# Optimization experiments

Hardware: AMD Instinct MI355X
Metric: run time of the kernel (lower is better)

Reference implementation:

```python
import jax, jax.numpy as jnp
import numpy as np

T = 100000
M = 32
PI_CONST = 3.1415926  # matches the constant used in the original source


def setup_inputs() -> dict:
    key = jax.random.key(0)
    k1, k2, k3, k4, k5, k6 = jax.random.split(key, 6)
    obs_2_T = jax.random.normal(k1, (T,), dtype=jnp.float32)
    obs_1_T_1 = jax.random.normal(k2, (T,), dtype=jnp.float32)
    mean = jax.random.normal(k3, (M,), dtype=jnp.float32)
    # variances must be positive
    var = jax.random.uniform(k4, (M,), dtype=jnp.float32) + jnp.float32(0.5)
    bate = jnp.float32(0.85)
    # pi: valid initial distribution; aij: row-stochastic transition matrix
    pi = jax.nn.softmax(jax.random.normal(k5, (M,), dtype=jnp.float32))
    aij = jax.nn.softmax(jax.random.normal(k6, (M, M), dtype=jnp.float32), axis=-1)
    return {"obs_2_T": obs_2_T, "obs_1_T_1": obs_1_T_1, "mean": mean,
            "var": var, "bate": bate, "pi": pi, "aij": aij}


def reference(obs_2_T, obs_1_T_1, mean, var, bate, pi, aij):
    # Eta[i, j, t] = exp(-(obs2[t] - (mean[j] + bate*(obs1[t] - mean[i]))) / (2*var[j]))
    #               / sqrt(2*pi*var[j])
    # (NOTE: faithful to the source, which does NOT square the residual.)
    inv2v = 1.0 / (2.0 * var)                      # (m,)
    norm = 1.0 / jnp.sqrt(2.0 * PI_CONST * var)    # (m,)
    # diff: (m_i, m_j, T)
    diff = obs_2_T[None, None, :] - (mean[None, :, None]
                                     + bate * (obs_1_T_1[None, None, :] - mean[:, None, None]))
    Eta = jnp.exp(-diff * inv2v[None, :, None]) * norm[None, :, None]  # (m, m, T)
    Eta_t = jnp.moveaxis(Eta, -1, 0)  # (T, m, m)

    # Normalized forward recursion:
    # t=0: num[i,j] = Eta[i,j,0] * pi[i] * aij[i,j]
    # t>0: num[i,j] = Eta[i,j,t] * Epsilon[t-1,i] * aij[i,j]
    # Gamma[t] = num / sum(num);  Epsilon[t,j] = sum_i Gamma[t,i,j]
    def step(eps_prev, eta):  # eps_prev: (m,), eta: (m, m)
        num = eta * eps_prev[:, None] * aij
        g = num / jnp.sum(num)
        return jnp.sum(g, axis=0), g

    _, Gamma = jax.lax.scan(step, pi, Eta_t)  # Gamma: (T, m, m)

    # loss = sum_t <Gamma[t], Eta[:, :, t]>
    loss = jnp.sum(Gamma * Eta_t)
    return loss
```

## Files before the change

### kernel.cpp

```cpp
#include <hip/hip_runtime.h>

constexpr int TN   = 100000;
constexpr int NCH  = 2000;
constexpr int CLEN = 50;
constexpr int WARM = 12;
constexpr int WPB  = 4;
constexpr int NBLK = NCH / WPB;
constexpr int MAXS = WARM + CLEN;

constexpr float LOG2E = 1.4426950408889634f;
constexpr float PI_F  = 3.1415926f;

typedef float v2f __attribute__((ext_vector_type(2)));

#define ROR(src, N) __int_as_float(__builtin_amdgcn_mov_dpp( \
    __float_as_int(src), 0x120 + (N), 0xF, 0xF, false))

#define RING16(v) { v += ROR(v,1); v += ROR(v,2); v += ROR(v,4); v += ROR(v,8); }

#define ROTPAIRS(SRC, P)                                                      \
  v2f P[8];                                                                   \
  { P[0] = (v2f){SRC,        ROR(SRC,1)};  P[1] = (v2f){ROR(SRC,2),  ROR(SRC,3)};  \
    P[2] = (v2f){ROR(SRC,4), ROR(SRC,5)};  P[3] = (v2f){ROR(SRC,6),  ROR(SRC,7)};  \
    P[4] = (v2f){ROR(SRC,8), ROR(SRC,9)};  P[5] = (v2f){ROR(SRC,10), ROR(SRC,11)}; \
    P[6] = (v2f){ROR(SRC,12),ROR(SRC,13)}; P[7] = (v2f){ROR(SRC,14), ROR(SRC,15)}; }

#define PKDOT(Wp, P, dd)                                                      \
  float dd;                                                                   \
  { v2f a0 = Wp[0]*P[0], a1 = Wp[1]*P[1], a2 = Wp[2]*P[2], a3 = Wp[3]*P[3];   \
    a0 += Wp[4]*P[4]; a1 += Wp[5]*P[5]; a2 += Wp[6]*P[6]; a3 += Wp[7]*P[7];   \
    v2f b = (a0 + a1) + (a2 + a3);                                            \
    dd = b.x + b.y; }

__global__ __launch_bounds__(256, 5) void k_main(
    const float* __restrict__ obs2, const float* __restrict__ obs1,
    const float* __restrict__ mean_p, const float* __restrict__ var_p,
    const float* __restrict__ bate_p, const float* __restrict__ pi_p,
    const float* __restrict__ aij, float* __restrict__ out)
{
  const int w = threadIdx.x >> 6, lane = threadIdx.x & 63;
  const int wv = blockIdx.x * WPB + w;
  const int i  = lane & 15;
  const int b4 = (lane >> 4) & 1;
  const int h  = lane >> 5;
  const int j  = lane & 31;
  const int kb = h * 16;
  const int m  = kb + i;
  const int idx1 = m, idx2 = m + 32;

  __shared__ __align__(16) float Wsh[2][32][32];
  __shared__ float cts[WPB][MAXS + 4];
  __shared__ float bsum[WPB];

  {
    const int tid = threadIdx.x;
    const int jj = tid & 31, ig = tid >> 5;
    float vjq  = var_p[jj];
    float i2vq = 0.5f / vjq;
    float norm = rsqrtf(2.0f * PI_F * vjq);
    float Aj   = norm * expf(mean_p[jj] * i2vq);
    float bate = bate_p[0];
#pragma unroll
    for (int mm = 0; mm < 4; ++mm) {
      int ii = ig * 4 + mm;
      float Bij = expf(-bate * mean_p[ii] * i2vq);
      float wq = aij[ii * 32 + jj] * Aj * Bij;
      Wsh[0][ii][jj] = wq;
      Wsh[1][ii][jj] = wq * Aj * Bij;
    }
  }

  float i2v_j = 0.5f / var_p[j];
  float s_ = i2v_j;
#pragma unroll
  for (int o = 1; o < 32; o <<= 1) s_ += __shfl_xor(s_, o);
  const float mbar    = s_ * 0.03125f;
  const float slope_m = (0.5f / var_p[m] - mbar) * LOG2E;
  const float Mc      = mbar * LOG2E;

  const int t0 = wv * CLEN;
  const int tw = (t0 > WARM) ? (t0 - WARM) : 0;
  const int n  = t0 + CLEN - tw;
  const int warmsteps = t0 - tw;
  {
    float bate = bate_p[0];
    for (int l = lane; l < n; l += 64)
      cts[w][l] = obs2[tw + l] - bate * obs1[tw + l];
  }
  __syncthreads();

  int dird;
  { int p = __builtin_amdgcn_mov_dpp(i, 0x121, 0xF, 0xF, false);
    dird = (p - i) & 15; }

  v2f Wp[8], Vp[8];
#pragma unroll
  for (int N = 0; N < 8; ++N) {
    int k0 = (i + (2 * N)     * dird) & 15;
    int k1 = (i + (2 * N + 1) * dird) & 15;
    Wp[N] = (v2f){Wsh[0][kb + k0][j], Wsh[0][kb + k1][j]};
    Vp[N] = (v2f){Wsh[1][kb + k0][j], Wsh[1][kb + k1][j]};
  }

  float ysrc = (tw == 0) ? pi_p[m] : 0.03125f;

  for (int s = 0; s < warmsteps; ++s) {
    float ct = cts[w][s];
    float uB = exp2f(-ct * slope_m);
    ROTPAIRS(ysrc, P)
    PKDOT(Wp, P, pW)
    float bA = __shfl(pW, idx1);
    float bB = __shfl(pW, idx2);
    ysrc = uB * (bA + bB);
    if ((s & 7) == 7)
      ysrc *= __builtin_amdgcn_rcpf(__int_as_float(
                __builtin_amdgcn_readfirstlane(__float_as_int(ysrc))));
  }
  float lossacc = 0.f;
#pragma unroll 4
  for (int q = 0; q < CLEN; ++q) {
    float ct   = cts[w][warmsteps + q];
    float uB   = exp2f(-ct * slope_m);
    float corr = exp2f(-ct * Mc);
    ROTPAIRS(ysrc, P)
    PKDOT(Wp, P, pW)
    PKDOT(Vp, P, pV)
    float bA = __shfl(pW, idx1);
    float bB = __shfl(pW, idx2);
    float cA = __shfl(pV, idx1);
    float cB = __shfl(pV, idx2);
    float ynew = uB * (bA + bB);
    float vV   = (uB * uB) * (cA + cB);
    ysrc = ynew;
    if ((q & 7) == 7)
      ysrc *= __builtin_amdgcn_rcpf(__int_as_float(
                __builtin_amdgcn_readfirstlane(__float_as_int(ysrc))));
    float red = b4 ? vV : ynew;
    RING16(red)
    red += __shfl_xor(red, 32);
    float cross = __shfl_xor(red, 16);
    float S  = b4 ? cross : red;
    float N2 = b4 ? red   : cross;
    lossacc += corr * N2 * __builtin_amdgcn_rcpf(S);
  }
  if (lane == 0) bsum[w] = lossacc;
  __syncthreads();
  if (threadIdx.x == 0)
    atomicAdd(out, (bsum[0] + bsum[1]) + (bsum[2] + bsum[3]));
}

extern "C" void kernel_launch(void* const* d_in, const int* in_sizes, int n_in,
                              void* d_out, int out_size, void* d_ws, size_t ws_size,
                              hipStream_t stream)
{
  (void)in_sizes; (void)n_in; (void)ws_size; (void)d_ws;
  const float* obs2 = (const float*)d_in[0];
  const float* obs1 = (const float*)d_in[1];
  const float* mean = (const float*)d_in[2];
  const float* var  = (const float*)d_in[3];
  const float* bate = (const float*)d_in[4];
  const float* pi   = (const float*)d_in[5];
  const float* aij  = (const float*)d_in[6];
  float* out = (float*)d_out;

  hipMemsetAsync(out, 0, sizeof(float) * out_size, stream);
  k_main<<<NBLK, 256, 0, stream>>>(obs2, obs1, mean, var, bate, pi, aij, out);
}
```

Before: 107.3 us.

## Interleave two independent time chunks per wave for ILP in forward recursion

Splits the sequence into twice as many shorter chunks and has each wave advance two independent chunks at once, so the serial shuffle/DPP dependency chains of one chunk can overlap with the other. The final cross-half reduction now uses readlane to scalar registers instead of two shuffles. Launch bounds drop to two blocks per CU minimum, allowing more registers per thread. Shorter chunks mean the warm-up steps make up a larger share of total work, and there are half as many waves to hide latency.

```diff
diff --git a/kernel.cpp b/kernel.cpp
--- a/kernel.cpp
+++ b/kernel.cpp
@@ -1,11 +1,13 @@
 #include <hip/hip_runtime.h>
 
 constexpr int TN   = 100000;
-constexpr int NCH  = 2000;
-constexpr int CLEN = 50;
+constexpr int NCH  = 4000;
+constexpr int CLEN = 25;
 constexpr int WARM = 12;
+constexpr int ILP  = 2;
+constexpr int NWAVE = NCH / ILP;
 constexpr int WPB  = 4;
-constexpr int NBLK = NCH / WPB;
+constexpr int NBLK = NWAVE / WPB;
 constexpr int MAXS = WARM + CLEN;
 
 constexpr float LOG2E = 1.4426950408889634f;
@@ -17,6 +19,11 @@
     __float_as_int(src), 0x120 + (N), 0xF, 0xF, false))
 
 #define RING16(v) { v += ROR(v,1); v += ROR(v,2); v += ROR(v,4); v += ROR(v,8); }
+
+#define RDL(x, L) __int_as_float(__builtin_amdgcn_readlane(__float_as_int(x), (L)))
+
+#define RENORM(y) y *= __builtin_amdgcn_rcpf(__int_as_float( \
+    __builtin_amdgcn_readfirstlane(__float_as_int(y))));
 
 #define ROTPAIRS(SRC, P)                                                      \
   v2f P[8];                                                                   \
@@ -32,7 +39,7 @@
     v2f b = (a0 + a1) + (a2 + a3);                                            \
     dd = b.x + b.y; }
 
-__global__ __launch_bounds__(256, 5) void k_main(
+__global__ __launch_bounds__(256, 2) void k_main(
     const float* __restrict__ obs2, const float* __restrict__ obs1,
     const float* __restrict__ mean_p, const float* __restrict__ var_p,
     const float* __restrict__ bate_p, const float* __restrict__ pi_p,
@@ -49,7 +56,7 @@
   const int idx1 = m, idx2 = m + 32;
 
   __shared__ __align__(16) float Wsh[2][32][32];
-  __shared__ float cts[WPB][MAXS + 4];
+  __shared__ float cts[WPB][ILP][MAXS + 3];
   __shared__ float bsum[WPB];
 
   {
@@ -78,14 +85,20 @@
   const float slope_m = (0.5f / var_p[m] - mbar) * LOG2E;
   const float Mc      = mbar * LOG2E;
 
-  const int t0 = wv * CLEN;
-  const int tw = (t0 > WARM) ? (t0 - WARM) : 0;
-  const int n  = t0 + CLEN - tw;
-  const int warmsteps = t0 - tw;
+  const int cA = wv,            cB = wv + NWAVE;
+  const int t0A = cA * CLEN,    t0B = cB * CLEN;
+  const int twA = (t0A > WARM) ? (t0A - WARM) : 0;
+  const int twB = t0B - WARM;
+  const int wsA = t0A - twA;
+  const int nA  = t0A + CLEN - twA;
+  const int nB  = WARM + CLEN;
+
   {
     float bate = bate_p[0];
-    for (int l = lane; l < n; l += 64)
-      cts[w][l] = obs2[tw + l] - bate * obs1[tw + l];
+    for (int l = lane; l < nA; l += 64)
+      cts[w][0][l] = obs2[twA + l] - bate * obs1[twA + l];
+    for (int l = lane; l < nB; l += 64)
+      cts[w][1][l] = obs2[twB + l] - bate * obs1[twB + l];
   }
   __syncthreads();
 
@@ -102,46 +115,65 @@
     Vp[N] = (v2f){Wsh[1][kb + k0][j], Wsh[1][kb + k1][j]};
   }
 
-  float ysrc = (tw == 0) ? pi_p[m] : 0.03125f;
-
-  for (int s = 0; s < warmsteps; ++s) {
-    float ct = cts[w][s];
-    float uB = exp2f(-ct * slope_m);
-    ROTPAIRS(ysrc, P)
-    PKDOT(Wp, P, pW)
-    float bA = __shfl(pW, idx1);
-    float bB = __shfl(pW, idx2);
-    ysrc = uB * (bA + bB);
-    if ((s & 7) == 7)
-      ysrc *= __builtin_amdgcn_rcpf(__int_as_float(
-                __builtin_amdgcn_readfirstlane(__float_as_int(ysrc))));
-  }
+  float ysA = (twA == 0) ? pi_p[m] : 0.03125f;
+  float ysB = 0.03125f;
+
+  for (int s = 0; s < WARM; ++s) {
+    if (wsA) {
+      float ct = cts[w][0][s];
+      float uB = exp2f(-ct * slope_m);
+      ROTPAIRS(ysA, PA)
+      PKDOT(Wp, PA, pW)
+      float a1 = __shfl(pW, idx1);
+      float a2 = __shfl(pW, idx2);
+      ysA = uB * (a1 + a2);
+      if ((s & 7) == 7) { RENORM(ysA) }
+    }
+    {
+      float ct = cts[w][1][s];
+      float uB = exp2f(-ct * slope_m);
+      ROTPAIRS(ysB, PB)
+      PKDOT(Wp, PB, pW)
+      float a1 = __shfl(pW, idx1);
+      float a2 = __shfl(pW, idx2);
+      ysB = uB * (a1 + a2);
+      if ((s & 7) == 7) { RENORM(ysB) }
+    }
+  }
+
   float lossacc = 0.f;
-#pragma unroll 4
+#pragma unroll 5
   for (int q = 0; q < CLEN; ++q) {
-    float ct   = cts[w][warmsteps + q];
-    float uB   = exp2f(-ct * slope_m);
-    float corr = exp2f(-ct * Mc);
-    ROTPAIRS(ysrc, P)
-    PKDOT(Wp, P, pW)
-    PKDOT(Vp, P, pV)
-    float bA = __shfl(pW, idx1);
-    float bB = __shfl(pW, idx2);
-    float cA = __shfl(pV, idx1);
-    float cB = __shfl(pV, idx2);
-    float ynew = uB * (bA + bB);
-    float vV   = (uB * uB) * (cA + cB);
-    ysrc = ynew;
-    if ((q & 7) == 7)
-      ysrc *= __builtin_amdgcn_rcpf(__int_as_float(
-                __builtin_amdgcn_readfirstlane(__float_as_int(ysrc))));
-    float red = b4 ? vV : ynew;
-    RING16(red)
-    red += __shfl_xor(red, 32);
-    float cross = __shfl_xor(red, 16);
-    float S  = b4 ? cross : red;
-    float N2 = b4 ? red   : cross;
-    lossacc += corr * N2 * __builtin_amdgcn_rcpf(S);
+    float ctA = cts[w][0][wsA + q];
+    float ctB = cts[w][1][WARM + q];
+    float uBA = exp2f(-ctA * slope_m), corrA = exp2f(-ctA * Mc);
+    float uBB = exp2f(-ctB * slope_m), corrB = exp2f(-ctB * Mc);
+    ROTPAIRS(ysA, PA)
+    ROTPAIRS(ysB, PB)
+    PKDOT(Wp, PA, pWA)
+    PKDOT(Vp, PA, pVA)
+    PKDOT(Wp, PB, pWB)
+    PKDOT(Vp, PB, pVB)
+    float bA1 = __shfl(pWA, idx1), bA2 = __shfl(pWA, idx2);
+    float cA1 = __shfl(pVA, idx1), cA2 = __shfl(pVA, idx2);
+    float bB1 = __shfl(pWB, idx1), bB2 = __shfl(pWB, idx2);
+    float cB1 = __shfl(pVB, idx1), cB2 = __shfl(pVB, idx2);
+    float ynA = uBA * (bA1 + bA2);
+    float vVA = (uBA * uBA) * (cA1 + cA2);
+    float ynB = uBB * (bB1 + bB2);
+    float vVB = (uBB * uBB) * (cB1 + cB2);
+    ysA = ynA; ysB = ynB;
+    if ((q & 7) == 7) { RENORM(ysA) RENORM(ysB) }
+    float redA = b4 ? vVA : ynA;
+    RING16(redA)
+    float SAv  = RDL(redA, 0)  + RDL(redA, 32);
+    float N2Av = RDL(redA, 16) + RDL(redA, 48);
+    lossacc += corrA * N2Av * __builtin_amdgcn_rcpf(SAv);
+    float redB = b4 ? vVB : ynB;
+    RING16(redB)
+    float SBv  = RDL(redB, 0)  + RDL(redB, 32);
+    float N2Bv = RDL(redB, 16) + RDL(redB, 48);
+    lossacc += corrB * N2Bv * __builtin_amdgcn_rcpf(SBv);
   }
   if (lane == 0) bsum[w] = lossacc;
   __syncthreads();
```

Result: faster. 90.59 us (-15.6%).

## Halve chunk length, double chunks, and reduce sums via readlane scalars

Applied to the files above, without the earlier changes.

Splits the time series into twice as many chunks of half the length, so each wavefront runs a shorter serial recursion and there are more wavefronts in flight. It replaces the final xor shuffles with readlane-based scalar sums, lowers launch-bounds occupancy from 5 to 4, and swaps the weight arrays for named scalar vector registers. The cost is that the fixed 12-step warmup is now spent on half as much useful work, adding redundant computation, and lower allowed occupancy may reduce latency hiding.

```diff
diff --git a/kernel.cpp b/kernel.cpp
--- a/kernel.cpp
+++ b/kernel.cpp
@@ -1,8 +1,8 @@
 #include <hip/hip_runtime.h>
 
 constexpr int TN   = 100000;
-constexpr int NCH  = 2000;
-constexpr int CLEN = 50;
+constexpr int NCH  = 4000;
+constexpr int CLEN = 25;
 constexpr int WARM = 12;
 constexpr int WPB  = 4;
 constexpr int NBLK = NCH / WPB;
@@ -18,21 +18,32 @@
 
 #define RING16(v) { v += ROR(v,1); v += ROR(v,2); v += ROR(v,4); v += ROR(v,8); }
 
-#define ROTPAIRS(SRC, P)                                                      \
-  v2f P[8];                                                                   \
-  { P[0] = (v2f){SRC,        ROR(SRC,1)};  P[1] = (v2f){ROR(SRC,2),  ROR(SRC,3)};  \
-    P[2] = (v2f){ROR(SRC,4), ROR(SRC,5)};  P[3] = (v2f){ROR(SRC,6),  ROR(SRC,7)};  \
-    P[4] = (v2f){ROR(SRC,8), ROR(SRC,9)};  P[5] = (v2f){ROR(SRC,10), ROR(SRC,11)}; \
-    P[6] = (v2f){ROR(SRC,12),ROR(SRC,13)}; P[7] = (v2f){ROR(SRC,14), ROR(SRC,15)}; }
+#define RDL(x, L) __int_as_float(__builtin_amdgcn_readlane(__float_as_int(x), (L)))
 
-#define PKDOT(Wp, P, dd)                                                      \
-  float dd;                                                                   \
-  { v2f a0 = Wp[0]*P[0], a1 = Wp[1]*P[1], a2 = Wp[2]*P[2], a3 = Wp[3]*P[3];   \
-    a0 += Wp[4]*P[4]; a1 += Wp[5]*P[5]; a2 += Wp[6]*P[6]; a3 += Wp[7]*P[7];   \
-    v2f b = (a0 + a1) + (a2 + a3);                                            \
-    dd = b.x + b.y; }
+#define RENORM(y) y *= __builtin_amdgcn_rcpf(__int_as_float( \
+    __builtin_amdgcn_readfirstlane(__float_as_int(y))));
 
-__global__ __launch_bounds__(256, 5) void k_main(
+#define ROTPAIRS8(SRC, p0,p1,p2,p3,p4,p5,p6,p7)                               \
+  v2f p0 = (v2f){SRC,         ROR(SRC,1)};                                    \
+  v2f p1 = (v2f){ROR(SRC,2),  ROR(SRC,3)};                                    \
+  v2f p2 = (v2f){ROR(SRC,4),  ROR(SRC,5)};                                    \
+  v2f p3 = (v2f){ROR(SRC,6),  ROR(SRC,7)};                                    \
+  v2f p4 = (v2f){ROR(SRC,8),  ROR(SRC,9)};                                    \
+  v2f p5 = (v2f){ROR(SRC,10), ROR(SRC,11)};                                   \
+  v2f p6 = (v2f){ROR(SRC,12), ROR(SRC,13)};                                   \
+  v2f p7 = (v2f){ROR(SRC,14), ROR(SRC,15)};
+
+static __device__ __forceinline__ float pkdot8(
+    v2f w0, v2f w1, v2f w2, v2f w3, v2f w4, v2f w5, v2f w6, v2f w7,
+    v2f p0, v2f p1, v2f p2, v2f p3, v2f p4, v2f p5, v2f p6, v2f p7)
+{
+  v2f a0 = w0*p0, a1 = w1*p1, a2 = w2*p2, a3 = w3*p3;
+  a0 += w4*p4; a1 += w5*p5; a2 += w6*p6; a3 += w7*p7;
+  v2f b = (a0 + a1) + (a2 + a3);
+  return b.x + b.y;
+}
+
+__global__ __launch_bounds__(256, 4) void k_main(
     const float* __restrict__ obs2, const float* __restrict__ obs1,
     const float* __restrict__ mean_p, const float* __restrict__ var_p,
     const float* __restrict__ bate_p, const float* __restrict__ pi_p,
@@ -49,7 +60,7 @@
   const int idx1 = m, idx2 = m + 32;
 
   __shared__ __align__(16) float Wsh[2][32][32];
-  __shared__ float cts[WPB][MAXS + 4];
+  __shared__ float cts[WPB][MAXS + 3];
   __shared__ float bsum[WPB];
 
   {
@@ -93,38 +104,42 @@
   { int p = __builtin_amdgcn_mov_dpp(i, 0x121, 0xF, 0xF, false);
     dird = (p - i) & 15; }
 
-  v2f Wp[8], Vp[8];
-#pragma unroll
-  for (int N = 0; N < 8; ++N) {
-    int k0 = (i + (2 * N)     * dird) & 15;
-    int k1 = (i + (2 * N + 1) * dird) & 15;
-    Wp[N] = (v2f){Wsh[0][kb + k0][j], Wsh[0][kb + k1][j]};
-    Vp[N] = (v2f){Wsh[1][kb + k0][j], Wsh[1][kb + k1][j]};
-  }
+  v2f w0, w1, w2, w3, w4, w5, w6, w7;
+  v2f q0, q1, q2, q3, q4, q5, q6, q7;
+#define LDW(N, WV, QV) {                                                      \
+    int k0 = (i + (2 * (N))     * dird) & 15;                                 \
+    int k1 = (i + (2 * (N) + 1) * dird) & 15;                                 \
+    WV = (v2f){Wsh[0][kb + k0][j], Wsh[0][kb + k1][j]};                       \
+    QV = (v2f){Wsh[1][kb + k0][j], Wsh[1][kb + k1][j]}; }
+  LDW(0, w0, q0) LDW(1, w1, q1) LDW(2, w2, q2) LDW(3, w3, q3)
+  LDW(4, w4, q4) LDW(5, w5, q5) LDW(6, w6, q6) LDW(7, w7, q7)
+#undef LDW
 
   float ysrc = (tw == 0) ? pi_p[m] : 0.03125f;
 
   for (int s = 0; s < warmsteps; ++s) {
     float ct = cts[w][s];
     float uB = exp2f(-ct * slope_m);
-    ROTPAIRS(ysrc, P)
-    PKDOT(Wp, P, pW)
-    float bA = __shfl(pW, idx1);
-    float bB = __shfl(pW, idx2);
-    ysrc = uB * (bA + bB);
-    if ((s & 7) == 7)
-      ysrc *= __builtin_amdgcn_rcpf(__int_as_float(
-                __builtin_amdgcn_readfirstlane(__float_as_int(ysrc))));
+    ROTPAIRS8(ysrc, p0, p1, p2, p3, p4, p5, p6, p7)
+    float pW = pkdot8(w0, w1, w2, w3, w4, w5, w6, w7,
+                      p0, p1, p2, p3, p4, p5, p6, p7);
+    float a1 = __shfl(pW, idx1);
+    float a2 = __shfl(pW, idx2);
+    ysrc = uB * (a1 + a2);
+    if ((s & 7) == 7) { RENORM(ysrc) }
   }
+
   float lossacc = 0.f;
-#pragma unroll 4
+#pragma unroll 5
   for (int q = 0; q < CLEN; ++q) {
     float ct   = cts[w][warmsteps + q];
     float uB   = exp2f(-ct * slope_m);
     float corr = exp2f(-ct * Mc);
-    ROTPAIRS(ysrc, P)
-    PKDOT(Wp, P, pW)
-    PKDOT(Vp, P, pV)
+    ROTPAIRS8(ysrc, p0, p1, p2, p3, p4, p5, p6, p7)
+    float pW = pkdot8(w0, w1, w2, w3, w4, w5, w6, w7,
+                      p0, p1, p2, p3, p4, p5, p6, p7);
+    float pV = pkdot8(q0, q1, q2, q3, q4, q5, q6, q7,
+                      p0, p1, p2, p3, p4, p5, p6, p7);
     float bA = __shfl(pW, idx1);
     float bB = __shfl(pW, idx2);
     float cA = __shfl(pV, idx1);
@@ -132,16 +147,12 @@
     float ynew = uB * (bA + bB);
     float vV   = (uB * uB) * (cA + cB);
     ysrc = ynew;
-    if ((q & 7) == 7)
-      ysrc *= __builtin_amdgcn_rcpf(__int_as_float(
-                __builtin_amdgcn_readfirstlane(__float_as_int(ysrc))));
+    if ((q & 7) == 7) { RENORM(ysrc) }
     float red = b4 ? vV : ynew;
     RING16(red)
-    red += __shfl_xor(red, 32);
-    float cross = __shfl_xor(red, 16);
-    float S  = b4 ? cross : red;
-    float N2 = b4 ? red   : cross;
-    lossacc += corr * N2 * __builtin_amdgcn_rcpf(S);
+    float Sv  = RDL(red, 0)  + RDL(red, 32);
+    float N2v = RDL(red, 16) + RDL(red, 48);
+    lossacc += corr * N2v * __builtin_amdgcn_rcpf(Sv);
   }
   if (lane == 0) bsum[w] = lossacc;
   __syncthreads();
```

Measured after the change: 90.11 us. -16.0%, faster.

## Remap state to 16 lanes with two elements each, dropping cross-lane shuffles

Applied to the files above, without the earlier changes.

Restructures the per-step matrix-vector product so each lane of a 16-lane row owns two state elements (i and i+16) and both output columns. The weights are held in registers as packed pairs, and rotated DPP reads feed broadcast packed FMAs. This removes the __shfl (ds_bpermute) gathers and the cross-half reductions on the serial dependency chain. It also normalizes every step instead of every eighth, and lowers the launch-bounds occupancy hint from 5 to 2 to fit the larger register footprint. The trade-offs are more DPP moves per step, more VGPRs, and less latency hiding from other waves.

```diff
diff --git a/kernel.cpp b/kernel.cpp
--- a/kernel.cpp
+++ b/kernel.cpp
@@ -18,21 +18,12 @@
 
 #define RING16(v) { v += ROR(v,1); v += ROR(v,2); v += ROR(v,4); v += ROR(v,8); }
 
-#define ROTPAIRS(SRC, P)                                                      \
-  v2f P[8];                                                                   \
-  { P[0] = (v2f){SRC,        ROR(SRC,1)};  P[1] = (v2f){ROR(SRC,2),  ROR(SRC,3)};  \
-    P[2] = (v2f){ROR(SRC,4), ROR(SRC,5)};  P[3] = (v2f){ROR(SRC,6),  ROR(SRC,7)};  \
-    P[4] = (v2f){ROR(SRC,8), ROR(SRC,9)};  P[5] = (v2f){ROR(SRC,10), ROR(SRC,11)}; \
-    P[6] = (v2f){ROR(SRC,12),ROR(SRC,13)}; P[7] = (v2f){ROR(SRC,14), ROR(SRC,15)}; }
+static __device__ __forceinline__ v2f sp(float x) { return (v2f){x, x}; }
 
-#define PKDOT(Wp, P, dd)                                                      \
-  float dd;                                                                   \
-  { v2f a0 = Wp[0]*P[0], a1 = Wp[1]*P[1], a2 = Wp[2]*P[2], a3 = Wp[3]*P[3];   \
-    a0 += Wp[4]*P[4]; a1 += Wp[5]*P[5]; a2 += Wp[6]*P[6]; a3 += Wp[7]*P[7];   \
-    v2f b = (a0 + a1) + (a2 + a3);                                            \
-    dd = b.x + b.y; }
+#define REP15(M) M(1) M(2) M(3) M(4) M(5) M(6) M(7) M(8) M(9) M(10) M(11) \
+                 M(12) M(13) M(14) M(15)
 
-__global__ __launch_bounds__(256, 5) void k_main(
+__global__ __launch_bounds__(256, 2) void k_main(
     const float* __restrict__ obs2, const float* __restrict__ obs1,
     const float* __restrict__ mean_p, const float* __restrict__ var_p,
     const float* __restrict__ bate_p, const float* __restrict__ pi_p,
@@ -41,15 +32,9 @@
   const int w = threadIdx.x >> 6, lane = threadIdx.x & 63;
   const int wv = blockIdx.x * WPB + w;
   const int i  = lane & 15;
-  const int b4 = (lane >> 4) & 1;
-  const int h  = lane >> 5;
-  const int j  = lane & 31;
-  const int kb = h * 16;
-  const int m  = kb + i;
-  const int idx1 = m, idx2 = m + 32;
 
   __shared__ __align__(16) float Wsh[2][32][32];
-  __shared__ float cts[WPB][MAXS + 4];
+  __shared__ float cts[WPB][MAXS + 2];
   __shared__ float bsum[WPB];
 
   {
@@ -70,13 +55,14 @@
     }
   }
 
-  float i2v_j = 0.5f / var_p[j];
-  float s_ = i2v_j;
-#pragma unroll
-  for (int o = 1; o < 32; o <<= 1) s_ += __shfl_xor(s_, o);
-  const float mbar    = s_ * 0.03125f;
-  const float slope_m = (0.5f / var_p[m] - mbar) * LOG2E;
-  const float Mc      = mbar * LOG2E;
+  float iva = 0.5f / var_p[i];
+  float ivb = 0.5f / var_p[i + 16];
+  float s2 = iva + ivb;
+  RING16(s2)
+  const float mbar = s2 * 0.03125f;
+  const float sx = (iva - mbar) * LOG2E;
+  const float sy = (ivb - mbar) * LOG2E;
+  const float Mc = mbar * LOG2E;
 
   const int t0 = wv * CLEN;
   const int tw = (t0 > WARM) ? (t0 - WARM) : 0;
@@ -93,56 +79,66 @@
   { int p = __builtin_amdgcn_mov_dpp(i, 0x121, 0xF, 0xF, false);
     dird = (p - i) & 15; }
 
-  v2f Wp[8], Vp[8];
-#pragma unroll
-  for (int N = 0; N < 8; ++N) {
-    int k0 = (i + (2 * N)     * dird) & 15;
-    int k1 = (i + (2 * N + 1) * dird) & 15;
-    Wp[N] = (v2f){Wsh[0][kb + k0][j], Wsh[0][kb + k1][j]};
-    Vp[N] = (v2f){Wsh[1][kb + k0][j], Wsh[1][kb + k1][j]};
-  }
+#define DECLW(d) v2f wa##d, wb##d, ua##d, ub##d;
+  DECLW(0) REP15(DECLW)
+#undef DECLW
+#define LOADW(d) {                                                            \
+    int k1 = (i + (d) * dird) & 15;                                           \
+    int k2 = k1 + 16;                                                         \
+    wa##d = (v2f){Wsh[0][k1][i], Wsh[0][k1][i + 16]};                         \
+    wb##d = (v2f){Wsh[0][k2][i], Wsh[0][k2][i + 16]};                         \
+    ua##d = (v2f){Wsh[1][k1][i], Wsh[1][k1][i + 16]};                         \
+    ub##d = (v2f){Wsh[1][k2][i], Wsh[1][k2][i + 16]}; }
+  LOADW(0) REP15(LOADW)
+#undef LOADW
 
-  float ysrc = (tw == 0) ? pi_p[m] : 0.03125f;
+  float Yx = (tw == 0) ? pi_p[i]      : 0.03125f;
+  float Yy = (tw == 0) ? pi_p[i + 16] : 0.03125f;
+
+#define WST(d) { float rx = ROR(Yx, d), ry = ROR(Yy, d);                      \
+    D0 += sp(rx) * wa##d; D1 += sp(ry) * wb##d; }
+#define MST(d) { float rx = ROR(Yx, d), ry = ROR(Yy, d);                      \
+    D0 += sp(rx) * wa##d; D1 += sp(ry) * wb##d;                               \
+    E0 += sp(rx) * ua##d; E1 += sp(ry) * ub##d; }
 
   for (int s = 0; s < warmsteps; ++s) {
     float ct = cts[w][s];
-    float uB = exp2f(-ct * slope_m);
-    ROTPAIRS(ysrc, P)
-    PKDOT(Wp, P, pW)
-    float bA = __shfl(pW, idx1);
-    float bB = __shfl(pW, idx2);
-    ysrc = uB * (bA + bB);
-    if ((s & 7) == 7)
-      ysrc *= __builtin_amdgcn_rcpf(__int_as_float(
-                __builtin_amdgcn_readfirstlane(__float_as_int(ysrc))));
+    float ex = exp2f(-ct * sx), ey = exp2f(-ct * sy);
+    v2f D0 = (v2f){0.f, 0.f}, D1 = (v2f){0.f, 0.f};
+    D0 += sp(Yx) * wa0; D1 += sp(Yy) * wb0;
+    REP15(WST)
+    v2f D = D0 + D1;
+    float ynx = ex * D.x, yny = ey * D.y;
+    float s_ = ynx + yny;
+    RING16(s_)
+    float r = __builtin_amdgcn_rcpf(s_);
+    Yx = ynx * r; Yy = yny * r;
   }
+
   float lossacc = 0.f;
-#pragma unroll 4
   for (int q = 0; q < CLEN; ++q) {
     float ct   = cts[w][warmsteps + q];
-    float uB   = exp2f(-ct * slope_m);
+    float ex = exp2f(-ct * sx), ey = exp2f(-ct * sy);
     float corr = exp2f(-ct * Mc);
-    ROTPAIRS(ysrc, P)
-    PKDOT(Wp, P, pW)
-    PKDOT(Vp, P, pV)
-    float bA = __shfl(pW, idx1);
-    float bB = __shfl(pW, idx2);
-    float cA = __shfl(pV, idx1);
-    float cB = __shfl(pV, idx2);
-    float ynew = uB * (bA + bB);
-    float vV   = (uB * uB) * (cA + cB);
-    ysrc = ynew;
-    if ((q & 7) == 7)
-      ysrc *= __builtin_amdgcn_rcpf(__int_as_float(
-                __builtin_amdgcn_readfirstlane(__float_as_int(ysrc))));
-    float red = b4 ? vV : ynew;
-    RING16(red)
-    red += __shfl_xor(red, 32);
-    float cross = __shfl_xor(red, 16);
-    float S  = b4 ? cross : red;
-    float N2 = b4 ? red   : cross;
-    lossacc += corr * N2 * __builtin_amdgcn_rcpf(S);
+    v2f D0 = (v2f){0.f, 0.f}, D1 = (v2f){0.f, 0.f};
+    v2f E0 = (v2f){0.f, 0.f}, E1 = (v2f){0.f, 0.f};
+    D0 += sp(Yx) * wa0; D1 += sp(Yy) * wb0;
+    E0 += sp(Yx) * ua0; E1 += sp(Yy) * ub0;
+    REP15(MST)
+    v2f D = D0 + D1, E = E0 + E1;
+    float ynx = ex * D.x,        yny = ey * D.y;
+    float vx  = (ex * ex) * E.x, vy  = (ey * ey) * E.y;
+    float s_ = ynx + yny;
+    RING16(s_)
+    float n_ = vx + vy;
+    RING16(n_)
+    float r = __builtin_amdgcn_rcpf(s_);
+    lossacc += corr * n_ * r;
+    Yx = ynx * r; Yy = yny * r;
   }
+#undef WST
+#undef MST
+
   if (lane == 0) bsum[w] = lossacc;
   __syncthreads();
   if (threadIdx.x == 0)
```

New measurement: 102.3 us. -4.7%, faster.
